# Kernel optimization log

Measured on AMD Instinct MI355X. Metric: run time of the kernel, lower is better.

## Reference

```python
import jax, jax.numpy as jnp
import numpy as np

LINK_LEN = 3
LN_EPS = 1e-5


def _layer_norm(x, w, b):
    mu = jnp.mean(x, axis=-1, keepdims=True)
    var = jnp.var(x, axis=-1, keepdims=True)
    return (x - mu) * jax.lax.rsqrt(var + LN_EPS) * w + b


def setup_inputs() -> dict:
    key = jax.random.key(0)
    ks = jax.random.split(key, 7)
    B, LAG, N, DIN, E, H = 16, 12, 5000, 32, 64, 64
    HH = H // 2
    return {
        "x": jax.random.normal(ks[0], (B, N, DIN), jnp.float32),
        "x_window": jax.random.normal(ks[1], (B, LAG, N, DIN // 2), jnp.float32),
        "node_embeddings": jax.random.normal(ks[2], (N, E), jnp.float32),
        "weights_pool": jax.random.normal(ks[3], (E, LINK_LEN, DIN, HH), jnp.float32) * 0.1,
        "weights_window": jax.random.normal(ks[4], (E, DIN // 2, HH), jnp.float32) * 0.1,
        "bias_pool": jax.random.normal(ks[5], (E, H), jnp.float32) * 0.1,
        "T": jax.random.normal(ks[6], (LAG,), jnp.float32),
        "ln1_w": jnp.ones((HH,), jnp.float32),
        "ln1_b": jnp.zeros((HH,), jnp.float32),
        "ln2_w": jnp.ones((HH,), jnp.float32),
        "ln2_b": jnp.zeros((HH,), jnp.float32),
    }


def reference(x, x_window, node_embeddings, weights_pool, weights_window,
              bias_pool, T, ln1_w, ln1_b, ln2_w, ln2_b):
    N = node_embeddings.shape[0]
    # adaptive adjacency: softmax(relu(E E^T)) over rows' neighbors (dim=1)
    supports = jax.nn.softmax(jax.nn.relu(node_embeddings @ node_embeddings.T), axis=1)
    support_set = [jnp.eye(N, dtype=x.dtype), supports]
    for k in range(2, LINK_LEN):
        support_set.append(supports @ support_set[k - 1])
    S = jnp.stack(support_set, axis=0)                      # [k, N, N]
    # per-node dynamic weights / bias from embeddings
    weights = jnp.einsum('nd,dkio->nkio', node_embeddings, weights_pool)  # [N,k,DIN,HH]
    bias = node_embeddings @ bias_pool                                     # [N,H]
    # graph conv path
    x_g = jnp.einsum('knm,bmc->bnkc', S, x)                 # [B,N,k,DIN]
    x_gconv = jnp.einsum('bnki,nkio->bno', x_g, weights)    # [B,N,HH]
    # temporal window path
    ww = jnp.einsum('nd,dio->nio', node_embeddings, weights_window)        # [N,DIN/2,HH]
    x_w = jnp.einsum('btni,nio->bnot', x_window, ww)        # [B,N,HH,LAG]
    x_wconv = x_w @ T                                       # [B,N,HH]
    out = jnp.concatenate([_layer_norm(x_gconv, ln1_w, ln1_b),
                           _layer_norm(x_wconv, ln2_w, ln2_b)], axis=-1) + bias
    return out
```

## Files before the change

kernel.cpp:

```cpp
#include <hip/hip_runtime.h>
#include <hip/hip_bf16.h>

#define NN   5000
#define EDIM 64
#define DINC 32
#define BB   16
#define LAGN 12
#define BC   512
#define KPAD 5120

typedef __attribute__((ext_vector_type(8))) short short8;
typedef __attribute__((ext_vector_type(4))) float float4v;

static __device__ __forceinline__ ushort f2bf(float x) {
  __hip_bfloat16 h = __float2bfloat16(x);
  return *reinterpret_cast<ushort*>(&h);
}
static __device__ __forceinline__ float bf2f(ushort u) {
  unsigned int x = ((unsigned int)u) << 16;
  return __uint_as_float(x);
}
static __device__ __forceinline__ short8 cvt8(const float* p) {
  const float4 v0 = *(const float4*)p, v1 = *(const float4*)(p + 4);
  short8 r;
  r[0] = (short)f2bf(v0.x); r[1] = (short)f2bf(v0.y);
  r[2] = (short)f2bf(v0.z); r[3] = (short)f2bf(v0.w);
  r[4] = (short)f2bf(v1.x); r[5] = (short)f2bf(v1.y);
  r[6] = (short)f2bf(v1.z); r[7] = (short)f2bf(v1.w);
  return r;
}

static __device__ __forceinline__ void gll16(const ushort* g, ushort* l) {
  __builtin_amdgcn_global_load_lds(
      (const __attribute__((address_space(1))) void*)g,
      (__attribute__((address_space(3))) void*)l, 16, 0, 0);
}


__global__ __launch_bounds__(256) void prep_kernel(const float* __restrict__ x,
                                                   const float* __restrict__ wpool,
                                                   const float* __restrict__ wwin,
                                                   const float* __restrict__ emb,
                                                   ushort* __restrict__ XbT,
                                                   float* __restrict__ wpP,
                                                   float* __restrict__ wwP,
                                                   ushort* __restrict__ eH,
                                                   ushort* __restrict__ eL) {
  const int b = blockIdx.x, tid = threadIdx.x;
  if (b < 10240) {
    const int j = b / 20, m = (b - j * 20) * 256 + tid;
    const int bb = j >> 5, c = j & 31;
    ushort v = 0;
    if (m < NN) v = f2bf(x[((size_t)bb * NN + m) * DINC + c]);
    XbT[(size_t)j * KPAD + m] = v;
  } else if (b < 11008) {
    const int t = (b - 10240) * 256 + tid;
    const int d = t / 3072, r = t - d * 3072;
    const int kk = r >> 10, r2 = r & 1023, i = r2 >> 5, o = r2 & 31;
    wpP[(size_t)d * 3072 + o * 96 + kk * 32 + i] = wpool[t];
  } else if (b < 11136) {
    const int t = (b - 11008) * 256 + tid;
    const int d = t >> 9, r = t & 511, i = r >> 5, o = r & 31;
    wwP[(size_t)d * 512 + o * 16 + i] = wwin[t];
  } else {
    const int t = (b - 11136) * 256 + tid;
    const int row = t >> 6;
    float v = 0.f;
    if (row < NN) v = emb[t];
    const ushort h = f2bf(v);
    eH[t] = h;
    eL[t] = f2bf(v - bf2f(h));
  }
}

__global__ __launch_bounds__(256) void fused_A_softmax_kernel(const ushort* __restrict__ eH,
                                                              const ushort* __restrict__ eL,
                                                              ushort* __restrict__ P,
                                                              ushort* __restrict__ scr) {
  const int tid = threadIdx.x;
  const int w = tid >> 6, l = tid & 63;
  const int fm = l & 15, kq = l >> 4;
  const int rg = blockIdx.x >> 2, ch = blockIdx.x & 3;
  const int row0 = rg * 32;
  const int cw = w * 64 + fm;
  __shared__ float redL[4][32];
  __shared__ float diagL[32];

  short8 aH[2][2], aL[2][2];
#pragma unroll
  for (int mf = 0; mf < 2; ++mf)
#pragma unroll
    for (int s = 0; s < 2; ++s) {
      const size_t o = (size_t)(row0 + mf * 16 + fm) * 64 + (s * 4 + kq) * 8;
      aH[mf][s] = *(const short8*)(eH + o);
      aL[mf][s] = *(const short8*)(eL + o);
    }

#pragma unroll
  for (int mf = 0; mf < 2; ++mf) {
    float p = 0.f;
#pragma unroll
    for (int s = 0; s < 2; ++s)
#pragma unroll
      for (int j = 0; j < 8; ++j) {
        const float v = bf2f((ushort)aH[mf][s][j]) + bf2f((ushort)aL[mf][s][j]);
        p = fmaf(v, v, p);
      }
    p += __shfl_xor(p, 16);
    p += __shfl_xor(p, 32);
    if (w == 0 && kq == 0) diagL[mf * 16 + fm] = p;
  }
  __syncthreads();
  float shift[2][4];
#pragma unroll
  for (int mf = 0; mf < 2; ++mf)
#pragma unroll
    for (int r = 0; r < 4; ++r) shift[mf][r] = diagL[mf * 16 + kq * 4 + r];

  float rs[2][4] = {};
  ushort* prow[2][4];
#pragma unroll
  for (int mf = 0; mf < 2; ++mf)
#pragma unroll
    for (int r = 0; r < 4; ++r) {
      const int gm = row0 + mf * 16 + kq * 4 + r;
      prow[mf][r] = (gm < NN) ? (P + (size_t)gm * 10000 + (gm & 1) * 16) : scr;
    }
  for (int t = 0; t < 5; ++t) {
    const int c0 = ch * 1280 + t * 256;
    short8 bH[4][2], bL[4][2];
#pragma unroll
    for (int nf = 0; nf < 4; ++nf)
#pragma unroll
      for (int s = 0; s < 2; ++s) {
        const size_t o = (size_t)(c0 + cw + nf * 16) * 64 + (s * 4 + kq) * 8;
        bH[nf][s] = *(const short8*)(eH + o);
        bL[nf][s] = *(const short8*)(eL + o);
      }
    float4v acc[2][4] = {};
#pragma unroll
    for (int s = 0; s < 2; ++s)
#pragma unroll
      for (int mf = 0; mf < 2; ++mf)
#pragma unroll
        for (int nf = 0; nf < 4; ++nf) {
          acc[mf][nf] = __builtin_amdgcn_mfma_f32_16x16x32_bf16(aL[mf][s], bH[nf][s], acc[mf][nf], 0, 0, 0);
          acc[mf][nf] = __builtin_amdgcn_mfma_f32_16x16x32_bf16(aH[mf][s], bL[nf][s], acc[mf][nf], 0, 0, 0);
          acc[mf][nf] = __builtin_amdgcn_mfma_f32_16x16x32_bf16(aH[mf][s], bH[nf][s], acc[mf][nf], 0, 0, 0);
        }
#pragma unroll
    for (int nf = 0; nf < 4; ++nf) {
      const int col = c0 + cw + nf * 16;
      const bool ok = col < NN;
#pragma unroll
      for (int mf = 0; mf < 2; ++mf)
#pragma unroll
        for (int r = 0; r < 4; ++r) {
          const float v = fmaxf(acc[mf][nf][r], 0.f);
          const float e = ok ? __expf(v - shift[mf][r]) : 0.f;
          rs[mf][r] += e;
          prow[mf][r][col] = f2bf(e);
        }
    }
  }
#pragma unroll
  for (int mf = 0; mf < 2; ++mf)
#pragma unroll
    for (int r = 0; r < 4; ++r) {
      float v = rs[mf][r];
#pragma unroll
      for (int msk = 1; msk < 16; msk <<= 1) v += __shfl_xor(v, msk);
      rs[mf][r] = v;
    }
  if (fm == 0) {
#pragma unroll
    for (int mf = 0; mf < 2; ++mf)
#pragma unroll
      for (int r = 0; r < 4; ++r) redL[w][mf * 16 + kq * 4 + r] = rs[mf][r];
  }
  __syncthreads();
  if (w == 0 && fm == 0) {
#pragma unroll
    for (int mf = 0; mf < 2; ++mf)
#pragma unroll
      for (int r = 0; r < 4; ++r) {
        const int mm = mf * 16 + kq * 4 + r;
        const int gm = row0 + mm;
        if (gm < NN) {
          const float tot = redL[0][mm] + redL[1][mm] + redL[2][mm] + redL[3][mm];
          *(float*)(P + (size_t)gm * 10000 + 9472 + 2 * ch) = tot;
        }
      }
  }
}

__global__ __launch_bounds__(256) void mfma_gemm_kernel(const ushort* __restrict__ Pm,
                                                        const ushort* __restrict__ Bt,
                                                        ushort* __restrict__ Pp) {
  __shared__ __align__(16) ushort Ls[32768];
  const int tid = threadIdx.x;
  const int w = tid >> 6, l = tid & 63;
  const int fm = l & 15, kq = l >> 4;
  const int wm = w >> 1, wn = w & 1;
  const int id = blockIdx.x;
  const int xb = id / 320;
  const int rr = id - xb * 320;
  const int yb = rr >> 3;
  const int zb = rr & 7;
  const int row0 = yb * 128, col0 = xb * 128;
  const int kbase = zb * 640;
  const int rstg = tid >> 3;
  const int slot = tid & 7;
  const ushort* gAq[4];
  const ushort* gBq[4];
#pragma unroll
  for (int q = 0; q < 4; ++q) {
    const int r = q * 32 + rstg;
    const int cg = slot ^ (r & 7);
    const int arow = row0 + r;
    gAq[q] = Pm + (size_t)arow * 10000 + (arow & 1) * 16 + kbase + cg * 8;
    gBq[q] = Bt + (size_t)(col0 + r) * KPAD + kbase + cg * 8;
  }
  ushort* lA = Ls + tid * 8;
  ushort* lB = Ls + 8192 + tid * 8;
  float4v acc[4][4] = {};

  auto stage = [&](int buf) {
#pragma unroll
    for (int q = 0; q < 4; ++q) gll16(gAq[q], lA + buf * 16384 + q * 2048);
#pragma unroll
    for (int q = 0; q < 4; ++q) gll16(gBq[q], lB + buf * 16384 + q * 2048);
#pragma unroll
    for (int q = 0; q < 4; ++q) { gAq[q] += 64; gBq[q] += 64; }
  };
  auto compute = [&](int buf) {
    const ushort* As = Ls + buf * 16384;
    const ushort* Bs = As + 8192;
#pragma unroll
    for (int s = 0; s < 2; ++s) {
      short8 a[4], b[4];
#pragma unroll
      for (int mt = 0; mt < 4; ++mt) {
        const int row = wm * 64 + mt * 16 + fm;
        const int sl = (s * 4 + kq) ^ (fm & 7);
        a[mt] = *(const short8*)(As + row * 64 + sl * 8);
      }
#pragma unroll
      for (int nt = 0; nt < 4; ++nt) {
        const int row = wn * 64 + nt * 16 + fm;
        const int sl = (s * 4 + kq) ^ (fm & 7);
        b[nt] = *(const short8*)(Bs + row * 64 + sl * 8);
      }
#pragma unroll
      for (int mt = 0; mt < 4; ++mt)
#pragma unroll
        for (int nt = 0; nt < 4; ++nt)
          acc[mt][nt] = __builtin_amdgcn_mfma_f32_16x16x32_bf16(a[mt], b[nt], acc[mt][nt], 0, 0, 0);
    }
  };

  stage(0);
  __syncthreads();
  int cur = 0;
  for (int kt = 0; kt < 9; ++kt) {
    stage(cur ^ 1);
    compute(cur);
    __syncthreads();
    cur ^= 1;
  }
  compute(cur);

  const int cb = col0 + wn * 64 + fm;
  const int zoff = 5160 + zb * 512;
#pragma unroll
  for (int mt = 0; mt < 4; ++mt)
#pragma unroll
    for (int r = 0; r < 4; ++r) {
      const int gm = row0 + wm * 64 + mt * 16 + kq * 4 + r;
      if (gm < NN) {
        ushort* prow = Pp + (size_t)gm * 10000 + zoff + cb;
#pragma unroll
        for (int nt = 0; nt < 4; ++nt) prow[nt * 16] = f2bf(acc[mt][nt][r]);
      }
    }
}

__global__ __launch_bounds__(256) void reduce_kernel(const ushort* __restrict__ Pp,
                                                     float* __restrict__ Yf,
                                                     ushort* __restrict__ Yt,
                                                     int writeT) {
  const int m0 = blockIdx.y * 64, n0 = blockIdx.x * 64;
  __shared__ __align__(16) ushort Lt[64][80];
  const int tid = threadIdx.x;
  const int mi = tid >> 4, nl4 = (tid & 15) << 2;
#pragma unroll
  for (int s = 0; s < 4; ++s) {
    const int m = m0 + mi + s * 16;
    float4 sum = make_float4(0.f, 0.f, 0.f, 0.f);
    if (m < NN) {
      const ushort* pr = Pp + (size_t)m * 10000 + 5160 + n0 + nl4;
#pragma unroll
      for (int z = 0; z < 8; ++z) {
        ushort4 u = *(const ushort4*)(pr + z * 512);
        sum.x += bf2f(u.x); sum.y += bf2f(u.y);
        sum.z += bf2f(u.z); sum.w += bf2f(u.w);
      }
      const float4 s4 = *(const float4*)(Pp + (size_t)m * 10000 + 9472);
      const float sc = 1.f / (s4.x + s4.y + s4.z + s4.w);
      sum.x *= sc; sum.y *= sc; sum.z *= sc; sum.w *= sc;
      *(float4*)(Yf + (size_t)m * BC + n0 + nl4) = sum;
    }
    if (writeT) {
      const int ml = mi + s * 16;
      Lt[nl4 + 0][ml] = f2bf(sum.x);
      Lt[nl4 + 1][ml] = f2bf(sum.y);
      Lt[nl4 + 2][ml] = f2bf(sum.z);
      Lt[nl4 + 3][ml] = f2bf(sum.w);
    }
  }
  if (writeT) {
    __syncthreads();
#pragma unroll
    for (int i = 0; i < 2; ++i) {
      const int g = tid + i * 256;
      const int nl = g >> 3, gi = g & 7;
      *(uint4*)(Yt + (size_t)(n0 + nl) * KPAD + m0 + gi * 8) =
          *(const uint4*)(&Lt[nl][gi * 8]);
    }
  }
}

__global__ __launch_bounds__(256) void emb_gemm_bf16_kernel(const float* __restrict__ Ae,
                                                            const float* __restrict__ Bp,
                                                            ushort* __restrict__ C,
                                                            int Nc) {
  __shared__ float Aet[EDIM][33];
  __shared__ __align__(16) float Bs[EDIM][64];
  const int row0 = blockIdx.y * 32, col0 = blockIdx.x * 64;
  const int tid = threadIdx.x;
  for (int i = tid; i < 512; i += 256) {
    const int r = i >> 4, d4 = (i & 15) << 2;
    const int gm = row0 + r;
    float4 v = make_float4(0.f, 0.f, 0.f, 0.f);
    if (gm < NN) v = *(const float4*)(Ae + (size_t)gm * EDIM + d4);
    Aet[d4 + 0][r] = v.x; Aet[d4 + 1][r] = v.y; Aet[d4 + 2][r] = v.z; Aet[d4 + 3][r] = v.w;
  }
  for (int i = tid; i < 1024; i += 256) {
    const int br = i >> 4, bc = (i & 15) << 2;
    *(float4*)&Bs[br][bc] = *(const float4*)(Bp + (size_t)br * Nc + col0 + bc);
  }
  __syncthreads();
  const int ty = tid >> 4, tx = tid & 15;
  float acc[2][4] = {};
#pragma unroll 8
  for (int d = 0; d < EDIM; ++d) {
    const float a0 = Aet[d][ty * 2], a1 = Aet[d][ty * 2 + 1];
    const float4 b4 = *(const float4*)&Bs[d][tx << 2];
    acc[0][0] = fmaf(a0, b4.x, acc[0][0]); acc[0][1] = fmaf(a0, b4.y, acc[0][1]);
    acc[0][2] = fmaf(a0, b4.z, acc[0][2]); acc[0][3] = fmaf(a0, b4.w, acc[0][3]);
    acc[1][0] = fmaf(a1, b4.x, acc[1][0]); acc[1][1] = fmaf(a1, b4.y, acc[1][1]);
    acc[1][2] = fmaf(a1, b4.z, acc[1][2]); acc[1][3] = fmaf(a1, b4.w, acc[1][3]);
  }
#pragma unroll
  for (int r = 0; r < 2; ++r) {
    const int gm = row0 + ty * 2 + r;
    if (gm >= NN) continue;
    ushort4 o4;
    o4.x = f2bf(acc[r][0]); o4.y = f2bf(acc[r][1]);
    o4.z = f2bf(acc[r][2]); o4.w = f2bf(acc[r][3]);
    *(ushort4*)(C + (size_t)gm * Nc + col0 + (tx << 2)) = o4;
  }
}

__global__ __launch_bounds__(256) void emb_gemm_kernel(const float* __restrict__ Ae,
                                                       const float* __restrict__ Bw,
                                                       float* __restrict__ C,
                                                       int M, int Nc) {
  __shared__ float Aet[EDIM][33];
  __shared__ __align__(16) float Bs[EDIM][64];
  const int row0 = blockIdx.y * 32, col0 = blockIdx.x * 64;
  const int tid = threadIdx.x;
  for (int i = tid; i < 512; i += 256) {
    const int r = i >> 4, d4 = (i & 15) << 2;
    const int gm = row0 + r;
    float4 v = make_float4(0.f, 0.f, 0.f, 0.f);
    if (gm < M) v = *(const float4*)(Ae + (size_t)gm * EDIM + d4);
    Aet[d4 + 0][r] = v.x; Aet[d4 + 1][r] = v.y; Aet[d4 + 2][r] = v.z; Aet[d4 + 3][r] = v.w;
  }
  for (int i = tid; i < 1024; i += 256) {
    const int br = i >> 4, bc = (i & 15) << 2;
    if (bc < Nc) *(float4*)&Bs[br][bc] = *(const float4*)(Bw + (size_t)br * Nc + bc);
  }
  __syncthreads();
  const int ty = tid >> 4, tx = tid & 15;
  float acc[2][4] = {};
#pragma unroll 8
  for (int d = 0; d < EDIM; ++d) {
    const float a0 = Aet[d][ty * 2], a1 = Aet[d][ty * 2 + 1];
    const float4 b4 = *(const float4*)&Bs[d][tx << 2];
    acc[0][0] = fmaf(a0, b4.x, acc[0][0]); acc[0][1] = fmaf(a0, b4.y, acc[0][1]);
    acc[0][2] = fmaf(a0, b4.z, acc[0][2]); acc[0][3] = fmaf(a0, b4.w, acc[0][3]);
    acc[1][0] = fmaf(a1, b4.x, acc[1][0]); acc[1][1] = fmaf(a1, b4.y, acc[1][1]);
    acc[1][2] = fmaf(a1, b4.z, acc[1][2]); acc[1][3] = fmaf(a1, b4.w, acc[1][3]);
  }
#pragma unroll
  for (int r = 0; r < 2; ++r) {
    const int gm = row0 + ty * 2 + r;
    if (gm >= M) continue;
    float4 o;
    o.x = acc[r][0]; o.y = acc[r][1]; o.z = acc[r][2]; o.w = acc[r][3];
    *(float4*)(C + (size_t)gm * Nc + col0 + (tx << 2)) = o;
  }
}

__global__ __launch_bounds__(256) void window_combine_kernel(const float* __restrict__ xw,
                                                             const float* __restrict__ T,
                                                             float* __restrict__ out) {
  const int idx = blockIdx.x * 256 + threadIdx.x;
  if (idx >= BB * NN * 16) return;
  const int b = idx / (NN * 16);
  const int rem = idx - b * (NN * 16);
  float acc = 0.f;
#pragma unroll
  for (int t = 0; t < LAGN; ++t)
    acc = fmaf(T[t], xw[(size_t)(b * LAGN + t) * (NN * 16) + rem], acc);
  out[idx] = acc;
}

__global__ __launch_bounds__(256) void fuse_mfma_kernel(const float* __restrict__ x,
                                                        const float* __restrict__ Y1f,
                                                        const float* __restrict__ Y2f,
                                                        const ushort* __restrict__ Wt,
                                                        const ushort* __restrict__ wwt,
                                                        const float* __restrict__ biasN,
                                                        const float* __restrict__ xwc,
                                                        const float* __restrict__ ln1w,
                                                        const float* __restrict__ ln1b,
                                                        const float* __restrict__ ln2w,
                                                        const float* __restrict__ ln2b,
                                                        float* __restrict__ out) {
  const int tid = threadIdx.x;
  const int n = blockIdx.x * 4 + (tid >> 6);
  const int l = tid & 63, fm = l & 15, kq = l >> 4;
  const short8 ax = cvt8(x + ((size_t)fm * NN + n) * DINC + kq * 8);
  const short8 a1 = cvt8(Y1f + (size_t)n * BC + fm * 32 + kq * 8);
  const short8 a2 = cvt8(Y2f + (size_t)n * BC + fm * 32 + kq * 8);
  short8 aw = {};
  if (kq < 2) aw = cvt8(xwc + ((size_t)fm * NN + n) * 16 + kq * 8);
  const ushort* wn = Wt + (size_t)n * 3072;
  const ushort* wwn = wwt + (size_t)n * 512;
  float4v accG[2] = {}, accW[2] = {};
#pragma unroll
  for (int t = 0; t < 2; ++t) {
    const int ob = (t * 16 + fm) * 96 + kq * 8;
    const short8 b0 = *(const short8*)(wn + ob);
    const short8 b1 = *(const short8*)(wn + ob + 32);
    const short8 b2 = *(const short8*)(wn + ob + 64);
    accG[t] = __builtin_amdgcn_mfma_f32_16x16x32_bf16(ax, b0, accG[t], 0, 0, 0);
    accG[t] = __builtin_amdgcn_mfma_f32_16x16x32_bf16(a1, b1, accG[t], 0, 0, 0);
    accG[t] = __builtin_amdgcn_mfma_f32_16x16x32_bf16(a2, b2, accG[t], 0, 0, 0);
    short8 bw = {};
    if (kq < 2) bw = *(const short8*)(wwn + (t * 16 + fm) * 16 + kq * 8);
    accW[t] = __builtin_amdgcn_mfma_f32_16x16x32_bf16(aw, bw, accW[t], 0, 0, 0);
  }
  const float w1a = ln1w[fm], w1b = ln1w[16 + fm];
  const float c1a = ln1b[fm], c1b = ln1b[16 + fm];
  const float w2a = ln2w[fm], w2b = ln2w[16 + fm];
  const float c2a = ln2b[fm], c2b = ln2b[16 + fm];
  const float* bn = biasN + (size_t)n * 64;
  const float bga = bn[fm], bgb = bn[16 + fm];
  const float bwa = bn[32 + fm], bwb = bn[48 + fm];
#pragma unroll
  for (int r = 0; r < 4; ++r) {
    const int b = kq * 4 + r;
    const float g0 = accG[0][r], g1 = accG[1][r];
    float s1 = g0 + g1, s2 = g0 * g0 + g1 * g1;
#pragma unroll
    for (int m = 1; m < 16; m <<= 1) { s1 += __shfl_xor(s1, m); s2 += __shfl_xor(s2, m); }
    const float mu = s1 * 0.03125f;
    const float rs = rsqrtf(s2 * 0.03125f - mu * mu + 1e-5f);
    const float h0 = accW[0][r], h1 = accW[1][r];
    float t1 = h0 + h1, t2 = h0 * h0 + h1 * h1;
#pragma unroll
    for (int m = 1; m < 16; m <<= 1) { t1 += __shfl_xor(t1, m); t2 += __shfl_xor(t2, m); }
    const float mu2 = t1 * 0.03125f;
    const float rs2 = rsqrtf(t2 * 0.03125f - mu2 * mu2 + 1e-5f);
    float* op = out + ((size_t)b * NN + n) * 64;
    op[fm]      = (g0 - mu) * rs * w1a + c1a + bga;
    op[16 + fm] = (g1 - mu) * rs * w1b + c1b + bgb;
    op[32 + fm] = (h0 - mu2) * rs2 * w2a + c2a + bwa;
    op[48 + fm] = (h1 - mu2) * rs2 * w2b + c2b + bwb;
  }
}

extern "C" void kernel_launch(void* const* d_in, const int* in_sizes, int n_in,
                              void* d_out, int out_size, void* d_ws, size_t ws_size,
                              hipStream_t stream) {
  const float* x     = (const float*)d_in[0];
  const float* xwin  = (const float*)d_in[1];
  const float* emb   = (const float*)d_in[2];
  const float* wpool = (const float*)d_in[3];
  const float* wwin  = (const float*)d_in[4];
  const float* bpool = (const float*)d_in[5];
  const float* T     = (const float*)d_in[6];
  const float* ln1w  = (const float*)d_in[7];
  const float* ln1b  = (const float*)d_in[8];
  const float* ln2w  = (const float*)d_in[9];
  const float* ln2b  = (const float*)d_in[10];
  float* out = (float*)d_out;
  float* ws = (float*)d_ws;

  ushort* P    = (ushort*)ws;
  ushort* XbT  = (ushort*)(ws + 25000000);
  ushort* Y1t  = (ushort*)(ws + 26310720);
  float*  Y1f  = ws + 27621440;
  float*  Y2f  = ws + 25000000;
  ushort* embH = (ushort*)(ws + 27621440);
  ushort* embL = (ushort*)(ws + 27785280);
  ushort* ascr = (ushort*)(ws + 27949120);
  ushort* Wt    = (ushort*)ws;
  ushort* wwt   = (ushort*)(ws + 15360000);
  float*  biasN = ws + 17920000;
  float*  xwc   = ws + 18240000;
  float*  wpP   = ws + 30181440;
  float*  wwP   = ws + 30378048;

  prep_kernel<<<12416, 256, 0, stream>>>(x, wpool, wwin, emb, XbT, wpP, wwP, embH, embL);
  fused_A_softmax_kernel<<<628, 256, 0, stream>>>(embH, embL, P, ascr);
  mfma_gemm_kernel<<<1280, 256, 0, stream>>>(P, XbT, P);
  reduce_kernel<<<dim3(8, 80), 256, 0, stream>>>(P, Y1f, Y1t, 1);
  mfma_gemm_kernel<<<1280, 256, 0, stream>>>(P, Y1t, P);
  reduce_kernel<<<dim3(8, 80), 256, 0, stream>>>(P, Y2f, (ushort*)nullptr, 0);
  emb_gemm_bf16_kernel<<<dim3(48, 157), 256, 0, stream>>>(emb, wpP, Wt, 3072);
  emb_gemm_bf16_kernel<<<dim3(8, 157), 256, 0, stream>>>(emb, wwP, wwt, 512);
  emb_gemm_kernel<<<dim3(1, 157), 256, 0, stream>>>(emb, bpool, biasN, NN, 64);
  window_combine_kernel<<<(BB * NN * 16 + 255) / 256, 256, 0, stream>>>(xwin, T, xwc);
  fuse_mfma_kernel<<<1250, 256, 0, stream>>>(x, Y1f, Y2f, Wt, wwt, biasN, xwc,
                                             ln1w, ln1b, ln2w, ln2b, out);
}
```

Before: 368.9 us.

## Double-buffer column embedding tiles in LDS for the fused A/softmax kernel

The column-side bf16 embedding tiles (high and low halves) are now staged into shared memory with direct global-to-LDS loads. Staging uses a double buffer with an XOR swizzle, and the next 128-column tile is prefetched while the current one runs through MFMA and exp. Previously each wave loaded its own B fragments straight from global memory into registers, one 256-column step at a time. The aim is to hide global load latency behind compute, at the cost of 64KB of LDS per block, which limits occupancy, plus an extra barrier on every iteration.

```diff
diff --git a/kernel.cpp b/kernel.cpp
--- a/kernel.cpp
+++ b/kernel.cpp
@@ -77,14 +77,36 @@
                                                               const ushort* __restrict__ eL,
                                                               ushort* __restrict__ P,
                                                               ushort* __restrict__ scr) {
+  __shared__ __align__(16) ushort Ls[32768];
   const int tid = threadIdx.x;
   const int w = tid >> 6, l = tid & 63;
   const int fm = l & 15, kq = l >> 4;
   const int rg = blockIdx.x >> 2, ch = blockIdx.x & 3;
   const int row0 = rg * 32;
-  const int cw = w * 64 + fm;
+  const int cbase = ch * 1280;
   __shared__ float redL[4][32];
   __shared__ float diagL[32];
+
+  const int rstg = tid >> 3;
+  const int slot = tid & 7;
+  ushort* lH = Ls + tid * 8;
+  ushort* lL = Ls + 8192 + tid * 8;
+
+  auto stage = [&](int buf, int t) {
+    const int c0 = cbase + t * 128;
+#pragma unroll
+    for (int q = 0; q < 4; ++q) {
+      const int r = q * 32 + rstg;
+      const int cg = slot ^ (r & 7);
+      gll16(eH + (size_t)(c0 + r) * 64 + cg * 8, lH + buf * 16384 + q * 2048);
+    }
+#pragma unroll
+    for (int q = 0; q < 4; ++q) {
+      const int r = q * 32 + rstg;
+      const int cg = slot ^ (r & 7);
+      gll16(eL + (size_t)(c0 + r) * 64 + cg * 8, lL + buf * 16384 + q * 2048);
+    }
+  };
 
   short8 aH[2][2], aL[2][2];
 #pragma unroll
@@ -96,6 +118,8 @@
       aL[mf][s] = *(const short8*)(eL + o);
     }
 
+  stage(0, 0);
+
 #pragma unroll
   for (int mf = 0; mf < 2; ++mf) {
     float p = 0.f;
@@ -126,31 +150,34 @@
       const int gm = row0 + mf * 16 + kq * 4 + r;
       prow[mf][r] = (gm < NN) ? (P + (size_t)gm * 10000 + (gm & 1) * 16) : scr;
     }
-  for (int t = 0; t < 5; ++t) {
-    const int c0 = ch * 1280 + t * 256;
-    short8 bH[4][2], bL[4][2];
-#pragma unroll
-    for (int nf = 0; nf < 4; ++nf)
-#pragma unroll
-      for (int s = 0; s < 2; ++s) {
-        const size_t o = (size_t)(c0 + cw + nf * 16) * 64 + (s * 4 + kq) * 8;
-        bH[nf][s] = *(const short8*)(eH + o);
-        bL[nf][s] = *(const short8*)(eL + o);
-      }
-    float4v acc[2][4] = {};
-#pragma unroll
-    for (int s = 0; s < 2; ++s)
+
+  auto compute = [&](int buf, int t) {
+    const ushort* H = Ls + buf * 16384;
+    const ushort* L = H + 8192;
+    const int c0 = cbase + t * 128;
+    float4v acc[2][2] = {};
+#pragma unroll
+    for (int s = 0; s < 2; ++s) {
+      short8 bh[2], bl[2];
+#pragma unroll
+      for (int nf = 0; nf < 2; ++nf) {
+        const int row = w * 32 + nf * 16 + fm;
+        const int sl = (s * 4 + kq) ^ (fm & 7);
+        bh[nf] = *(const short8*)(H + row * 64 + sl * 8);
+        bl[nf] = *(const short8*)(L + row * 64 + sl * 8);
+      }
 #pragma unroll
       for (int mf = 0; mf < 2; ++mf)
 #pragma unroll
-        for (int nf = 0; nf < 4; ++nf) {
-          acc[mf][nf] = __builtin_amdgcn_mfma_f32_16x16x32_bf16(aL[mf][s], bH[nf][s], acc[mf][nf], 0, 0, 0);
-          acc[mf][nf] = __builtin_amdgcn_mfma_f32_16x16x32_bf16(aH[mf][s], bL[nf][s], acc[mf][nf], 0, 0, 0);
-          acc[mf][nf] = __builtin_amdgcn_mfma_f32_16x16x32_bf16(aH[mf][s], bH[nf][s], acc[mf][nf], 0, 0, 0);
+        for (int nf = 0; nf < 2; ++nf) {
+          acc[mf][nf] = __builtin_amdgcn_mfma_f32_16x16x32_bf16(aL[mf][s], bh[nf], acc[mf][nf], 0, 0, 0);
+          acc[mf][nf] = __builtin_amdgcn_mfma_f32_16x16x32_bf16(aH[mf][s], bl[nf], acc[mf][nf], 0, 0, 0);
+          acc[mf][nf] = __builtin_amdgcn_mfma_f32_16x16x32_bf16(aH[mf][s], bh[nf], acc[mf][nf], 0, 0, 0);
         }
-#pragma unroll
-    for (int nf = 0; nf < 4; ++nf) {
-      const int col = c0 + cw + nf * 16;
+    }
+#pragma unroll
+    for (int nf = 0; nf < 2; ++nf) {
+      const int col = c0 + w * 32 + nf * 16 + fm;
       const bool ok = col < NN;
 #pragma unroll
       for (int mf = 0; mf < 2; ++mf)
@@ -162,7 +189,17 @@
           prow[mf][r][col] = f2bf(e);
         }
     }
-  }
+  };
+
+  int cur = 0;
+  for (int t = 0; t < 9; ++t) {
+    stage(cur ^ 1, t + 1);
+    compute(cur, t);
+    __syncthreads();
+    cur ^= 1;
+  }
+  compute(cur, 9);
+
 #pragma unroll
   for (int mf = 0; mf < 2; ++mf)
 #pragma unroll
@@ -172,6 +209,7 @@
       for (int msk = 1; msk < 16; msk <<= 1) v += __shfl_xor(v, msk);
       rs[mf][r] = v;
     }
+  __syncthreads();
   if (fm == 0) {
 #pragma unroll
     for (int mf = 0; mf < 2; ++mf)
```

After: 367.4 us. No clear change (-0.4%).
